# Kernel tuning notes

Hardware: AMD Instinct MI355X
Metric: run time of the kernel (lower is better)

The kernel has to match this reference:

```python
import jax, jax.numpy as jnp
import numpy as np

OUT_RANGE = 6.0
OUT_SHIFT = -3.0


def setup_inputs() -> dict:
    key = jax.random.key(0)
    ks = jax.random.split(key, 6)
    B, T = 128, 64
    A, V, X = 48, 48, 96
    PF = 128
    fdim = (A + 1) * (V + 1) * (X + 1)  # 232897
    return {
        "audio_h": jax.random.normal(ks[0], (B, T, A), jnp.float32),
        "video_h": jax.random.normal(ks[1], (B, T, V), jnp.float32),
        "text_h": jax.random.normal(ks[2], (B, T, X), jnp.float32),
        "W1": jax.random.normal(ks[3], (fdim, PF), jnp.float32) * 0.002,
        "b1": jnp.zeros((PF,), jnp.float32),
        "W2": jax.random.normal(ks[4], (PF, PF), jnp.float32) * 0.05,
        "b2": jnp.zeros((PF,), jnp.float32),
        "W3": jax.random.normal(ks[5], (PF, 1), jnp.float32) * 0.05,
        "b3": jnp.zeros((1,), jnp.float32),
    }


def reference(audio_h, video_h, text_h, W1, b1, W2, b2, W3, b3):
    B, T, A = audio_h.shape
    V = video_h.shape[-1]
    X = text_h.shape[-1]
    one = jnp.ones((B, T, 1), audio_h.dtype)
    a = jnp.concatenate([one, audio_h], axis=-1)  # [B,T,A+1]
    v = jnp.concatenate([one, video_h], axis=-1)  # [B,T,V+1]
    x = jnp.concatenate([one, text_h], axis=-1)   # [B,T,X+1]
    # per-timestep triple outer product, summed over t.
    # flatten order matches torch: audio slowest, then video, text fastest.
    av = jnp.einsum("bta,btv->btav", a, v).reshape(B, T, (A + 1) * (V + 1))
    fusion = jnp.einsum("btp,btx->bpx", av, x).reshape(B, -1)  # [B,(A+1)(V+1)(X+1)]
    # dropout is identity in eval mode
    h1 = jax.nn.relu(fusion @ W1 + b1)
    h2 = jax.nn.relu(h1 @ W2 + b2)
    out = jax.nn.sigmoid(h2 @ W3 + b3) * OUT_RANGE + OUT_SHIFT  # [B,1] in (-3,3)
    return out
```

## Files before the change

kernel.cpp:

```cpp
#include <hip/hip_runtime.h>


#define B_    128
#define T_    64
#define A1    49
#define V1    49
#define X1    97
#define IJ    2401
#define KTOT  232897
#define FP    232928
#define PF    128
#define KC    512
#define NB2   455

typedef short s8v __attribute__((ext_vector_type(8)));
typedef float f4v __attribute__((ext_vector_type(4)));

__device__ __forceinline__ unsigned short f2bf(float f) {
    union { float f; unsigned u; } v; v.f = f;
    return (unsigned short)((v.u + 0x7FFFu + ((v.u >> 16) & 1u)) >> 16);
}

__global__ __launch_bounds__(512) void k1_fusion(
    const float* __restrict__ audio, const float* __restrict__ video,
    const float* __restrict__ text, unsigned short* __restrict__ fusion)
{
    __shared__ float a_s[T_ * A1];
    __shared__ float v_s[T_ * V1];
    __shared__ unsigned short xT[112 * 72];
    __shared__ unsigned short w_ws[8][16 * 72];

    const int b = blockIdx.y;
    const int bx = blockIdx.x;
    const int tid = threadIdx.x;

    for (int idx = tid; idx < T_ * A1; idx += 512) {
        int t = idx / 49, i = idx - t * 49;
        a_s[idx] = (i == 0) ? 1.0f : audio[(b * T_ + t) * 48 + (i - 1)];
        v_s[idx] = (i == 0) ? 1.0f : video[(b * T_ + t) * 48 + (i - 1)];
    }
    for (int idx = tid; idx < T_ * X1; idx += 512) {
        int t = idx / 97, k = idx - t * 97;
        xT[k * 72 + t] = f2bf((k == 0) ? 1.0f : text[(b * T_ + t) * 96 + (k - 1)]);
    }
    for (int idx = tid; idx < 15 * 64; idx += 512) {
        xT[(97 + (idx >> 6)) * 72 + (idx & 63)] = 0;
    }
    if (bx == 0) {
        for (int idx = tid; idx < FP - KTOT; idx += 512)
            fusion[(size_t)b * FP + KTOT + idx] = 0;
    }
    __syncthreads();

    const int wave = tid >> 6, lane = tid & 63;
    const int q = lane >> 4, ln = lane & 15;
    unsigned short* w_s = w_ws[wave];

    for (int it = 0; it < 5; ++it) {
        const int tw = it * 8 + wave;
        if (tw >= 38) break;
        const int tl = bx * 38 + tw;
        if (tl >= 151) break;
        const int ij0 = tl * 16;

        #pragma unroll
        for (int ijl = 0; ijl < 16; ++ijl) {
            int ij = ij0 + ijl;
            unsigned short wv = 0;
            if (ij < IJ) {
                int i = ij / 49, j = ij - i * 49;
                wv = f2bf(a_s[lane * 49 + i] * v_s[lane * 49 + j]);
            }
            w_s[ijl * 72 + lane] = wv;
        }
        s8v af0 = *(const s8v*)&w_s[ln * 72 + q * 8];
        s8v af1 = *(const s8v*)&w_s[ln * 72 + 32 + q * 8];
        #pragma unroll
        for (int nt = 0; nt < 7; ++nt) {
            s8v bf0 = *(const s8v*)&xT[(nt * 16 + ln) * 72 + q * 8];
            s8v bf1 = *(const s8v*)&xT[(nt * 16 + ln) * 72 + 32 + q * 8];
            f4v acc = {0.f, 0.f, 0.f, 0.f};
            acc = __builtin_amdgcn_mfma_f32_16x16x32_bf16(af0, bf0, acc, 0, 0, 0);
            acc = __builtin_amdgcn_mfma_f32_16x16x32_bf16(af1, bf1, acc, 0, 0, 0);
            int kk = nt * 16 + ln;
            if (kk < X1) {
                #pragma unroll
                for (int r = 0; r < 4; ++r) {
                    int ij = ij0 + q * 4 + r;
                    if (ij < IJ)
                        fusion[(size_t)b * FP + ij * X1 + kk] = f2bf(acc[r]);
                }
            }
        }
    }
}

#define BPAD 40
__global__ __launch_bounds__(512) void k2_gemm(
    const unsigned short* __restrict__ fusion, const float* __restrict__ W1,
    float* __restrict__ partials)
{
    __shared__ unsigned short B_l[2][128 * BPAD];

    const int blk = blockIdx.x;
    const int kbase = blk * KC;
    const int nsteps = min(KC >> 5, (FP - kbase) >> 5);
    const int tid = threadIdx.x;
    const int wave = tid >> 6, lane = tid & 63;
    const int q = lane >> 4, ln = lane & 15;

    const int fB = tid & 127, g = tid >> 7;

    const unsigned short* Arow =
        fusion + (size_t)(wave * 16 + ln) * FP + kbase + q * 8;

    f4v acc[8];
    #pragma unroll
    for (int n = 0; n < 8; ++n) acc[n] = (f4v){0.f, 0.f, 0.f, 0.f};

    {
        float bv[8];
        #pragma unroll
        for (int c = 0; c < 8; ++c) {
            int p = kbase + g * 8 + c;
            bv[c] = (p < KTOT) ? W1[(size_t)p * PF + fB] : 0.f;
        }
        ushort4 lo, hi;
        lo.x = f2bf(bv[0]); lo.y = f2bf(bv[1]); lo.z = f2bf(bv[2]); lo.w = f2bf(bv[3]);
        hi.x = f2bf(bv[4]); hi.y = f2bf(bv[5]); hi.z = f2bf(bv[6]); hi.w = f2bf(bv[7]);
        *(ushort4*)&B_l[0][fB * BPAD + g * 8]     = lo;
        *(ushort4*)&B_l[0][fB * BPAD + g * 8 + 4] = hi;
    }
    s8v av = *(const s8v*)Arow;
    __syncthreads();

    for (int s = 0; s < nsteps; ++s) {
        const int cbuf = s & 1, nbuf = cbuf ^ 1;
        float bvn[8];
        s8v avn;
        const bool more = (s + 1 < nsteps);
        if (more) {
            const int p1 = kbase + (s + 1) * 32;
            #pragma unroll
            for (int c = 0; c < 8; ++c) {
                int p = p1 + g * 8 + c;
                bvn[c] = (p < KTOT) ? W1[(size_t)p * PF + fB] : 0.f;
            }
            avn = *(const s8v*)(Arow + (s + 1) * 32);
        }
        #pragma unroll
        for (int nt = 0; nt < 8; ++nt) {
            s8v bf = *(const s8v*)&B_l[cbuf][(nt * 16 + ln) * BPAD + q * 8];
            acc[nt] = __builtin_amdgcn_mfma_f32_16x16x32_bf16(av, bf, acc[nt], 0, 0, 0);
        }
        if (more) {
            ushort4 lo, hi;
            lo.x = f2bf(bvn[0]); lo.y = f2bf(bvn[1]); lo.z = f2bf(bvn[2]); lo.w = f2bf(bvn[3]);
            hi.x = f2bf(bvn[4]); hi.y = f2bf(bvn[5]); hi.z = f2bf(bvn[6]); hi.w = f2bf(bvn[7]);
            *(ushort4*)&B_l[nbuf][fB * BPAD + g * 8]     = lo;
            *(ushort4*)&B_l[nbuf][fB * BPAD + g * 8 + 4] = hi;
            av = avn;
        }
        __syncthreads();
    }

    float* outp = partials + (size_t)blk * (128 * 128);
    #pragma unroll
    for (int nt = 0; nt < 8; ++nt) {
        const int f = nt * 16 + ln;
        #pragma unroll
        for (int r = 0; r < 4; ++r)
            outp[(wave * 16 + q * 4 + r) * 128 + f] = acc[nt][r];
    }
}

__global__ __launch_bounds__(512) void k3_reduce(
    const float* __restrict__ partials, const float* __restrict__ b1,
    float* __restrict__ h1)
{
    __shared__ float red[512];
    const int e = blockIdx.x * 64 + (threadIdx.x & 63);
    const int rh = threadIdx.x >> 6;
    float s = 0.f;
    for (int r = rh; r < NB2; r += 8)
        s += partials[(size_t)r * 16384 + e];
    red[threadIdx.x] = s;
    __syncthreads();
    if (threadIdx.x < 64) {
        float v = 0.f;
        #pragma unroll
        for (int j = 0; j < 8; ++j) v += red[threadIdx.x + 64 * j];
        v += b1[e & 127];
        h1[e] = fmaxf(v, 0.f);
    }
}

__global__ __launch_bounds__(128) void k4_out(
    const float* __restrict__ h1, const float* __restrict__ W2,
    const float* __restrict__ b2, const float* __restrict__ W3,
    const float* __restrict__ b3, float* __restrict__ out)
{
    __shared__ float hrow[128];
    __shared__ float red2[2];
    const int b = blockIdx.x, f = threadIdx.x;
    hrow[f] = h1[b * 128 + f];
    __syncthreads();
    float s = b2[f];
    #pragma unroll 8
    for (int c = 0; c < 128; ++c) s += hrow[c] * W2[c * 128 + f];
    float p = fmaxf(s, 0.f) * W3[f];
    #pragma unroll
    for (int off = 32; off; off >>= 1) p += __shfl_down(p, off, 64);
    if ((f & 63) == 0) red2[f >> 6] = p;
    __syncthreads();
    if (f == 0) {
        float t = red2[0] + red2[1] + b3[0];
        out[b] = 6.0f / (1.0f + expf(-t)) - 3.0f;
    }
}

extern "C" void kernel_launch(void* const* d_in, const int* in_sizes, int n_in,
                              void* d_out, int out_size, void* d_ws, size_t ws_size,
                              hipStream_t stream)
{
    const float* audio = (const float*)d_in[0];
    const float* video = (const float*)d_in[1];
    const float* text  = (const float*)d_in[2];
    const float* W1 = (const float*)d_in[3];
    const float* b1 = (const float*)d_in[4];
    const float* W2 = (const float*)d_in[5];
    const float* b2 = (const float*)d_in[6];
    const float* W3 = (const float*)d_in[7];
    const float* b3 = (const float*)d_in[8];
    float* out = (float*)d_out;

    char* ws = (char*)d_ws;
    unsigned short* fusion = (unsigned short*)ws;
    float* partials = (float*)(ws + 59629568);
    float* h1 = (float*)(ws + 89448448);

    k1_fusion<<<dim3(4, 128), 512, 0, stream>>>(audio, video, text, fusion);
    k2_gemm<<<dim3(NB2), 512, 0, stream>>>(fusion, W1, partials);
    k3_reduce<<<dim3(256), 512, 0, stream>>>(partials, b1, h1);
    k4_out<<<dim3(128), 128, 0, stream>>>(h1, W2, b2, W3, b3, out);
}
```

Baseline: 256.6 us.

## Stage fusion tiles in LDS for coalesced stores; reschedule GEMM prefetch pipeline

In the fusion kernel, each wave now writes its 16x97 bf16 output tile into LDS and then copies it to global memory with contiguous 16-byte stores. This replaces the scattered 2-byte stores of the old code. The video features are kept as bf16 in LDS, and the i/j indices are stepped incrementally instead of recomputed with divisions. The GEMM kernel's K loop is unrolled into a fixed two-stage ping-pong with register prefetch of W1 two steps ahead. The last block now always runs 16 steps and reads fusion data past the padded row, relying on zeroed W1 values to cancel it. Rounding video to bf16 before the multiply slightly changes precision.

```diff
diff --git a/kernel.cpp b/kernel.cpp
--- a/kernel.cpp
+++ b/kernel.cpp
@@ -20,15 +20,19 @@
     union { float f; unsigned u; } v; v.f = f;
     return (unsigned short)((v.u + 0x7FFFu + ((v.u >> 16) & 1u)) >> 16);
 }
+__device__ __forceinline__ float bf2f(unsigned short h) {
+    union { unsigned u; float f; } v; v.u = ((unsigned)h) << 16;
+    return v.f;
+}
 
 __global__ __launch_bounds__(512) void k1_fusion(
     const float* __restrict__ audio, const float* __restrict__ video,
     const float* __restrict__ text, unsigned short* __restrict__ fusion)
 {
     __shared__ float a_s[T_ * A1];
-    __shared__ float v_s[T_ * V1];
+    __shared__ unsigned short v_s[T_ * V1];
     __shared__ unsigned short xT[112 * 72];
-    __shared__ unsigned short w_ws[8][16 * 72];
+    __shared__ unsigned short w_ws[8][1552];
 
     const int b = blockIdx.y;
     const int bx = blockIdx.x;
@@ -37,7 +41,7 @@
     for (int idx = tid; idx < T_ * A1; idx += 512) {
         int t = idx / 49, i = idx - t * 49;
         a_s[idx] = (i == 0) ? 1.0f : audio[(b * T_ + t) * 48 + (i - 1)];
-        v_s[idx] = (i == 0) ? 1.0f : video[(b * T_ + t) * 48 + (i - 1)];
+        v_s[idx] = f2bf((i == 0) ? 1.0f : video[(b * T_ + t) * 48 + (i - 1)]);
     }
     for (int idx = tid; idx < T_ * X1; idx += 512) {
         int t = idx / 97, k = idx - t * 97;
@@ -63,18 +67,21 @@
         if (tl >= 151) break;
         const int ij0 = tl * 16;
 
-        #pragma unroll
-        for (int ijl = 0; ijl < 16; ++ijl) {
-            int ij = ij0 + ijl;
-            unsigned short wv = 0;
-            if (ij < IJ) {
-                int i = ij / 49, j = ij - i * 49;
-                wv = f2bf(a_s[lane * 49 + i] * v_s[lane * 49 + j]);
+        {
+            int i = ij0 / 49, j = ij0 - (ij0 / 49) * 49;
+            #pragma unroll
+            for (int ijl = 0; ijl < 16; ++ijl) {
+                unsigned short wv = 0;
+                if (ij0 + ijl < IJ)
+                    wv = f2bf(a_s[lane * 49 + i] * bf2f(v_s[lane * 49 + j]));
+                w_s[ijl * 72 + lane] = wv;
+                if (++j == 49) { j = 0; ++i; }
             }
-            w_s[ijl * 72 + lane] = wv;
         }
         s8v af0 = *(const s8v*)&w_s[ln * 72 + q * 8];
         s8v af1 = *(const s8v*)&w_s[ln * 72 + 32 + q * 8];
+
+        f4v pacc[7];
         #pragma unroll
         for (int nt = 0; nt < 7; ++nt) {
             s8v bf0 = *(const s8v*)&xT[(nt * 16 + ln) * 72 + q * 8];
@@ -82,15 +89,28 @@
             f4v acc = {0.f, 0.f, 0.f, 0.f};
             acc = __builtin_amdgcn_mfma_f32_16x16x32_bf16(af0, bf0, acc, 0, 0, 0);
             acc = __builtin_amdgcn_mfma_f32_16x16x32_bf16(af1, bf1, acc, 0, 0, 0);
+            pacc[nt] = acc;
+        }
+
+        #pragma unroll
+        for (int nt = 0; nt < 7; ++nt) {
             int kk = nt * 16 + ln;
             if (kk < X1) {
                 #pragma unroll
-                for (int r = 0; r < 4; ++r) {
-                    int ij = ij0 + q * 4 + r;
-                    if (ij < IJ)
-                        fusion[(size_t)b * FP + ij * X1 + kk] = f2bf(acc[r]);
-                }
+                for (int r = 0; r < 4; ++r)
+                    w_s[(q * 4 + r) * 97 + kk] = f2bf(pacc[nt][r]);
             }
+        }
+        asm volatile("s_waitcnt lgkmcnt(0)" ::: "memory");
+        __builtin_amdgcn_sched_barrier(0);
+
+        const int nv = min(16, IJ - ij0);
+        const int bytes = nv * 194;
+        char* gdst = (char*)(fusion + (size_t)b * FP + (size_t)ij0 * 97);
+        const char* lsrc = (const char*)w_s;
+        for (int off = lane * 16; off < bytes; off += 1024) {
+            uint4 d = *(const uint4*)(lsrc + off);
+            *(uint4*)(gdst + off) = d;
         }
     }
 }
@@ -104,11 +124,9 @@
 
     const int blk = blockIdx.x;
     const int kbase = blk * KC;
-    const int nsteps = min(KC >> 5, (FP - kbase) >> 5);
     const int tid = threadIdx.x;
     const int wave = tid >> 6, lane = tid & 63;
     const int q = lane >> 4, ln = lane & 15;
-
     const int fB = tid & 127, g = tid >> 7;
 
     const unsigned short* Arow =
@@ -118,51 +136,63 @@
     #pragma unroll
     for (int n = 0; n < 8; ++n) acc[n] = (f4v){0.f, 0.f, 0.f, 0.f};
 
-    {
-        float bv[8];
-        #pragma unroll
-        for (int c = 0; c < 8; ++c) {
-            int p = kbase + g * 8 + c;
-            bv[c] = (p < KTOT) ? W1[(size_t)p * PF + fB] : 0.f;
-        }
-        ushort4 lo, hi;
-        lo.x = f2bf(bv[0]); lo.y = f2bf(bv[1]); lo.z = f2bf(bv[2]); lo.w = f2bf(bv[3]);
-        hi.x = f2bf(bv[4]); hi.y = f2bf(bv[5]); hi.z = f2bf(bv[6]); hi.w = f2bf(bv[7]);
-        *(ushort4*)&B_l[0][fB * BPAD + g * 8]     = lo;
-        *(ushort4*)&B_l[0][fB * BPAD + g * 8 + 4] = hi;
-    }
-    s8v av = *(const s8v*)Arow;
-    __syncthreads();
-
-    for (int s = 0; s < nsteps; ++s) {
-        const int cbuf = s & 1, nbuf = cbuf ^ 1;
-        float bvn[8];
-        s8v avn;
-        const bool more = (s + 1 < nsteps);
+#define LOADW(dst, s)                                                       \
+    {                                                                       \
+        _Pragma("unroll")                                                   \
+        for (int c = 0; c < 8; ++c) {                                       \
+            int p = kbase + (s) * 32 + g * 8 + c;                           \
+            dst[c] = (p < KTOT) ? W1[(size_t)p * PF + fB] : 0.f;            \
+        }                                                                   \
+    }
+#define PACKW(src, buf)                                                     \
+    {                                                                       \
+        ushort4 lo, hi;                                                     \
+        lo.x = f2bf(src[0]); lo.y = f2bf(src[1]);                           \
+        lo.z = f2bf(src[2]); lo.w = f2bf(src[3]);                           \
+        hi.x = f2bf(src[4]); hi.y = f2bf(src[5]);                           \
+        hi.z = f2bf(src[6]); hi.w = f2bf(src[7]);                           \
+        *(ushort4*)&B_l[buf][fB * BPAD + g * 8]     = lo;                   \
+        *(ushort4*)&B_l[buf][fB * BPAD + g * 8 + 4] = hi;                   \
+    }
+#define MFMA8(av, buf)                                                      \
+    {                                                                       \
+        _Pragma("unroll")                                                   \
+        for (int nt = 0; nt < 8; ++nt) {                                    \
+            s8v bfv = *(const s8v*)&B_l[buf][(nt * 16 + ln) * BPAD + q * 8];\
+            acc[nt] = __builtin_amdgcn_mfma_f32_16x16x32_bf16(              \
+                av, bfv, acc[nt], 0, 0, 0);                                 \
+        }                                                                   \
+    }
+
+    float w0[8], w1[8];
+    s8v a0v, a1v;
+
+    LOADW(w0, 0);
+    PACKW(w0, 0);
+    LOADW(w1, 1);
+    a0v = *(const s8v*)Arow;
+    __syncthreads();
+
+    for (int i = 0; i < 8; ++i) {
+        const bool more = (i < 7);
+        if (more) LOADW(w0, 2 * i + 2);
+        a1v = *(const s8v*)(Arow + (2 * i + 1) * 32);
+        MFMA8(a0v, 0);
+        PACKW(w1, 1);
+        __syncthreads();
         if (more) {
-            const int p1 = kbase + (s + 1) * 32;
-            #pragma unroll
-            for (int c = 0; c < 8; ++c) {
-                int p = p1 + g * 8 + c;
-                bvn[c] = (p < KTOT) ? W1[(size_t)p * PF + fB] : 0.f;
-            }
-            avn = *(const s8v*)(Arow + (s + 1) * 32);
-        }
-        #pragma unroll
-        for (int nt = 0; nt < 8; ++nt) {
-            s8v bf = *(const s8v*)&B_l[cbuf][(nt * 16 + ln) * BPAD + q * 8];
-            acc[nt] = __builtin_amdgcn_mfma_f32_16x16x32_bf16(av, bf, acc[nt], 0, 0, 0);
-        }
+            LOADW(w1, 2 * i + 3);
+            a0v = *(const s8v*)(Arow + (2 * i + 2) * 32);
+        }
+        MFMA8(a1v, 1);
         if (more) {
-            ushort4 lo, hi;
-            lo.x = f2bf(bvn[0]); lo.y = f2bf(bvn[1]); lo.z = f2bf(bvn[2]); lo.w = f2bf(bvn[3]);
-            hi.x = f2bf(bvn[4]); hi.y = f2bf(bvn[5]); hi.z = f2bf(bvn[6]); hi.w = f2bf(bvn[7]);
-            *(ushort4*)&B_l[nbuf][fB * BPAD + g * 8]     = lo;
-            *(ushort4*)&B_l[nbuf][fB * BPAD + g * 8 + 4] = hi;
-            av = avn;
-        }
-        __syncthreads();
-    }
+            PACKW(w0, 0);
+            __syncthreads();
+        }
+    }
+#undef LOADW
+#undef PACKW
+#undef MFMA8
 
     float* outp = partials + (size_t)blk * (128 * 128);
     #pragma unroll
```

Result: no change. 257.4 us (+0.3%).
